# Optimization experiments

Hardware: AMD Instinct MI355X
Metric: run time of the kernel (lower is better)

Reference implementation:

```python
import jax, jax.numpy as jnp
import numpy as np

N_NODES = 40000
N_EDGES = 640000
BATCH = 2
IN_DIM = 3
HID = 128
OUT_DIM = 3


def setup_inputs() -> dict:
    key = jax.random.key(0)
    ks = jax.random.split(key, 16)
    p = jax.random.normal(ks[0], (BATCH, N_NODES, IN_DIM), dtype=jnp.float32)
    edge_rows = jax.random.randint(ks[1], (N_EDGES,), 0, N_NODES, dtype=jnp.int32)
    edge_cols = jax.random.randint(ks[2], (N_EDGES,), 0, N_NODES, dtype=jnp.int32)
    # normalize_sparse_matrix: divide each nonzero (value 1.0) by the row's nonzero count
    deg = jax.ops.segment_sum(jnp.ones((N_EDGES,), jnp.float32), edge_rows, num_segments=N_NODES)
    adj_vals = 1.0 / deg[edge_rows]  # every used row has deg >= 1
    s = 0.05
    # initial Linear(3 -> 128)
    W_init = jax.random.normal(ks[3], (IN_DIM, HID), jnp.float32) * s
    b_init = jnp.zeros((HID,), jnp.float32)
    # 4 GraphConvs inside the two blocks (all 128->128), each has filter + self_filter
    Wf_blocks = jax.random.normal(ks[4], (4, HID, HID), jnp.float32) * s
    bf_blocks = jnp.zeros((4, HID), jnp.float32)
    Ws_blocks = jax.random.normal(ks[5], (4, HID, HID), jnp.float32) * s
    bs_blocks = jnp.zeros((4, HID), jnp.float32)
    # final GraphConvLayer (128 -> 3)
    Wf_out = jax.random.normal(ks[6], (HID, OUT_DIM), jnp.float32) * s
    bf_out = jnp.zeros((OUT_DIM,), jnp.float32)
    Ws_out = jax.random.normal(ks[7], (HID, OUT_DIM), jnp.float32) * s
    bs_out = jnp.zeros((OUT_DIM,), jnp.float32)
    return dict(p=p, adj_vals=adj_vals, edge_rows=edge_rows, edge_cols=edge_cols,
                W_init=W_init, b_init=b_init,
                Wf_blocks=Wf_blocks, bf_blocks=bf_blocks,
                Ws_blocks=Ws_blocks, bs_blocks=bs_blocks,
                Wf_out=Wf_out, bf_out=bf_out, Ws_out=Ws_out, bs_out=bs_out)


def reference(p, adj_vals, edge_rows, edge_cols,
              W_init, b_init,
              Wf_blocks, bf_blocks, Ws_blocks, bs_blocks,
              Wf_out, bf_out, Ws_out, bs_out):
    n = p.shape[1]

    def spmm(xb):  # xb: [N, d] -> A @ xb via edge-list scatter-add
        return jax.ops.segment_sum(adj_vals[:, None] * xb[edge_cols], edge_rows, num_segments=n)

    spmm_b = jax.vmap(spmm)  # [B, N, d]

    def gconv(x, Wf, bf, Ws, bs):
        # sparse path: self_filter(x) + filter(spmm(adj, x))
        return (x @ Ws + bs) + (spmm_b(x) @ Wf + bf)

    x = p @ W_init + b_init  # [B, N, HID]
    for blk in range(2):  # two GraphConvBlocks, residual, no shortcut (dims equal)
        net = gconv(jax.nn.relu(x), Wf_blocks[2 * blk], bf_blocks[2 * blk],
                    Ws_blocks[2 * blk], bs_blocks[2 * blk])
        dx = gconv(jax.nn.relu(net), Wf_blocks[2 * blk + 1], bf_blocks[2 * blk + 1],
                   Ws_blocks[2 * blk + 1], bs_blocks[2 * blk + 1])
        x = x + dx
    # final GraphConvLayer 128 -> 3
    out = gconv(jax.nn.relu(x), Wf_out, bf_out, Ws_out, bs_out)
    return out
```

## Files before the change

kernel.cpp:

```cpp
#include <hip/hip_runtime.h>


typedef unsigned short u16;
typedef unsigned int   u32;
typedef __bf16 bf8_t __attribute__((ext_vector_type(8)));
typedef float  f4_t  __attribute__((ext_vector_type(4)));

#define N_NODES 40000
#define N_EDGES 640000
#define BN      80000

__device__ __forceinline__ float bf2f(u16 u) {
  union { u32 i; float f; } v; v.i = ((u32)u) << 16; return v.f;
}
__device__ __forceinline__ u16 f2bf(float f) {
  union { float f; u32 i; } v; v.f = f;
  u32 i = v.i;
  return (u16)((i + 0x7FFFu + ((i >> 16) & 1u)) >> 16);
}
__device__ __forceinline__ float asf(u32 i) {
  union { u32 u; float f; } v; v.u = i; return v.f;
}
__device__ __forceinline__ u32 pack2(float a, float b) {
  return (u32)f2bf(a) | ((u32)f2bf(b) << 16);
}
__device__ __forceinline__ float lo2f(u32 v) { return asf(v << 16); }
__device__ __forceinline__ float hi2f(u32 v) { return asf(v & 0xffff0000u); }
__device__ __forceinline__ u32 relu2(u32 v) {
  u32 r = v;
  if (r & 0x8000u)     r &= 0xffff0000u;
  if (r & 0x80000000u) r &= 0x0000ffffu;
  return r;
}

__global__ void fill_kernel(float* __restrict__ out, int n, float v) {
  int i = blockIdx.x * 256 + threadIdx.x;
  if (i < n) out[i] = v;
}

__global__ void scan1_kernel(const int* __restrict__ cnt, int* __restrict__ row_ptr,
                             int* __restrict__ blocksum) {
  __shared__ int sm[256];
  int t = threadIdx.x;
  int row = blockIdx.x * 256 + t;
  int v = (row < N_NODES) ? cnt[row] : 0;
  sm[t] = v; __syncthreads();
  for (int off = 1; off < 256; off <<= 1) {
    int u = (t >= off) ? sm[t - off] : 0;
    __syncthreads();
    sm[t] += u;
    __syncthreads();
  }
  if (row < N_NODES) row_ptr[row] = sm[t] - v;
  if (t == 255) blocksum[blockIdx.x] = sm[255];
}

__global__ void scan2_kernel(int* __restrict__ blocksum, int* __restrict__ row_ptr, int nblk) {
  __shared__ int sm[256];
  int t = threadIdx.x;
  int v = (t < nblk) ? blocksum[t] : 0;
  sm[t] = v; __syncthreads();
  for (int off = 1; off < 256; off <<= 1) {
    int u = (t >= off) ? sm[t - off] : 0;
    __syncthreads();
    sm[t] += u;
    __syncthreads();
  }
  if (t < nblk) blocksum[t] = sm[t] - v;
  if (t == 255) row_ptr[N_NODES] = sm[255];
}

__global__ void scan3_kernel(int* __restrict__ row_ptr, const int* __restrict__ blocksum,
                             int* __restrict__ cnt) {
  int row = blockIdx.x * 256 + threadIdx.x;
  if (row < N_NODES) {
    int rp = row_ptr[row] + blocksum[blockIdx.x];
    row_ptr[row] = rp;
    cnt[row] = rp;
  }
}

__global__ void scatter_kernel(const int* __restrict__ rows, const int* __restrict__ cols,
                               int* __restrict__ cur, int* __restrict__ cols_s) {
  int e = blockIdx.x * 256 + threadIdx.x;
  if (e < N_EDGES) {
    int r = rows[e];
    int pos = atomicAdd(&cur[r], 1);
    cols_s[pos] = cols[e];
  }
}

__global__ void initw_kernel(const float* __restrict__ p, const float* __restrict__ W,
                             const float* __restrict__ bias, u16* __restrict__ xb,
                             const float* __restrict__ Wf_b, const float* __restrict__ Ws_b,
                             const float* __restrict__ bf_b, const float* __restrict__ bs_b,
                             u16* __restrict__ WtCat, float* __restrict__ biasCat,
                             const int* __restrict__ erows, int* __restrict__ cnt) {
  if (blockIdx.x >= 20512) {
    int e = (blockIdx.x - 20512) * 256 + threadIdx.x;
    if (e < N_EDGES) atomicAdd(&cnt[erows[e]], 1);
    return;
  }
  if (blockIdx.x >= 20000) {
    int idx = (blockIdx.x - 20000) * 256 + threadIdx.x;
    int g = idx >> 15, rem = idx & 32767;
    int h = rem >> 8, k = rem & 255;
    float v = (k < 128) ? Ws_b[(g * 128 + k) * 128 + h]
                        : Wf_b[(g * 128 + (k - 128)) * 128 + h];
    WtCat[idx] = f2bf(v);
    if (k == 0) biasCat[g * 128 + h] = bs_b[g * 128 + h] + bf_b[g * 128 + h];
    return;
  }
  int idx = blockIdx.x * 256 + threadIdx.x;
  int row = idx >> 6;
  int h = (idx & 63) * 2;
  float p0 = p[row * 3], p1 = p[row * 3 + 1], p2 = p[row * 3 + 2];
  float s0 = p0 * W[h]     + p1 * W[128 + h]     + p2 * W[256 + h]     + bias[h];
  float s1 = p0 * W[h + 1] + p1 * W[128 + h + 1] + p2 * W[256 + h + 1] + bias[h + 1];
  ((u32*)xb)[(size_t)row * 64 + (h >> 1)] = pack2(s0, s1);
}

#define ACC8P(u, a0, a1, a2, a3, a4, a5, a6, a7)                          \
  a0 += asf((u).x << 16); a1 += asf((u).x & 0xffff0000u);                 \
  a2 += asf((u).y << 16); a3 += asf((u).y & 0xffff0000u);                 \
  a4 += asf((u).z << 16); a5 += asf((u).z & 0xffff0000u);                 \
  a6 += asf((u).w << 16); a7 += asf((u).w & 0xffff0000u);

__global__ void spmm_plain(const int* __restrict__ row_ptr, const int* __restrict__ cols_s,
                           const u16* __restrict__ xin, u16* __restrict__ yout) {
  int row = blockIdx.x * 4 + (threadIdx.x >> 6);
  int l = threadIdx.x & 63;
  int g = l >> 4, sl = l & 15;
  int s = row_ptr[row], e = row_ptr[row + 1];
  const uint4* X0 = (const uint4*)xin + sl;
  const uint4* X1 = X0 + 640000;
  float a0 = 0.f, a1 = 0.f, a2 = 0.f, a3 = 0.f, a4 = 0.f, a5 = 0.f, a6 = 0.f, a7 = 0.f;
  float b0 = 0.f, b1 = 0.f, b2 = 0.f, b3 = 0.f, b4 = 0.f, b5 = 0.f, b6 = 0.f, b7 = 0.f;
  int i = s;
  for (; i + 7 < e; i += 8) {
    int c0 = cols_s[i + g], c1 = cols_s[i + 4 + g];
    uint4 u00 = X0[(size_t)c0 * 16];
    uint4 u01 = X1[(size_t)c0 * 16];
    uint4 u10 = X0[(size_t)c1 * 16];
    uint4 u11 = X1[(size_t)c1 * 16];
    ACC8P(u00, a0, a1, a2, a3, a4, a5, a6, a7);
    ACC8P(u01, b0, b1, b2, b3, b4, b5, b6, b7);
    ACC8P(u10, a0, a1, a2, a3, a4, a5, a6, a7);
    ACC8P(u11, b0, b1, b2, b3, b4, b5, b6, b7);
  }
  for (; i + 3 < e; i += 4) {
    int c = cols_s[i + g];
    uint4 u0 = X0[(size_t)c * 16];
    uint4 u1 = X1[(size_t)c * 16];
    ACC8P(u0, a0, a1, a2, a3, a4, a5, a6, a7);
    ACC8P(u1, b0, b1, b2, b3, b4, b5, b6, b7);
  }
  if (i + g < e) {
    int c = cols_s[i + g];
    uint4 u0 = X0[(size_t)c * 16];
    uint4 u1 = X1[(size_t)c * 16];
    ACC8P(u0, a0, a1, a2, a3, a4, a5, a6, a7);
    ACC8P(u1, b0, b1, b2, b3, b4, b5, b6, b7);
  }
  a0 += __shfl_xor(a0, 16); a1 += __shfl_xor(a1, 16); a2 += __shfl_xor(a2, 16); a3 += __shfl_xor(a3, 16);
  a4 += __shfl_xor(a4, 16); a5 += __shfl_xor(a5, 16); a6 += __shfl_xor(a6, 16); a7 += __shfl_xor(a7, 16);
  b0 += __shfl_xor(b0, 16); b1 += __shfl_xor(b1, 16); b2 += __shfl_xor(b2, 16); b3 += __shfl_xor(b3, 16);
  b4 += __shfl_xor(b4, 16); b5 += __shfl_xor(b5, 16); b6 += __shfl_xor(b6, 16); b7 += __shfl_xor(b7, 16);
  a0 += __shfl_xor(a0, 32); a1 += __shfl_xor(a1, 32); a2 += __shfl_xor(a2, 32); a3 += __shfl_xor(a3, 32);
  a4 += __shfl_xor(a4, 32); a5 += __shfl_xor(a5, 32); a6 += __shfl_xor(a6, 32); a7 += __shfl_xor(a7, 32);
  b0 += __shfl_xor(b0, 32); b1 += __shfl_xor(b1, 32); b2 += __shfl_xor(b2, 32); b3 += __shfl_xor(b3, 32);
  b4 += __shfl_xor(b4, 32); b5 += __shfl_xor(b5, 32); b6 += __shfl_xor(b6, 32); b7 += __shfl_xor(b7, 32);
  float sc = (e > s) ? 1.f / (float)(e - s) : 0.f;
  if (g == 0) {
    uint4 o;
    o.x = pack2(a0 * sc, a1 * sc);
    o.y = pack2(a2 * sc, a3 * sc);
    o.z = pack2(a4 * sc, a5 * sc);
    o.w = pack2(a6 * sc, a7 * sc);
    *((uint4*)yout + (size_t)row * 16 + sl) = o;
  } else if (g == 1) {
    uint4 o;
    o.x = pack2(b0 * sc, b1 * sc);
    o.y = pack2(b2 * sc, b3 * sc);
    o.z = pack2(b4 * sc, b5 * sc);
    o.w = pack2(b6 * sc, b7 * sc);
    *((uint4*)yout + 640000 + (size_t)row * 16 + sl) = o;
  }
}

#define ACC8M(u, a0, a1, a2, a3, a4, a5, a6, a7)                                        \
  a0 += fmaxf(asf((u).x << 16), 0.f); a1 += fmaxf(asf((u).x & 0xffff0000u), 0.f);       \
  a2 += fmaxf(asf((u).y << 16), 0.f); a3 += fmaxf(asf((u).y & 0xffff0000u), 0.f);       \
  a4 += fmaxf(asf((u).z << 16), 0.f); a5 += fmaxf(asf((u).z & 0xffff0000u), 0.f);       \
  a6 += fmaxf(asf((u).w << 16), 0.f); a7 += fmaxf(asf((u).w & 0xffff0000u), 0.f);

__global__ void spmm_relu(const int* __restrict__ row_ptr, const int* __restrict__ cols_s,
                          const u16* __restrict__ xin, u16* __restrict__ yout) {
  int row = blockIdx.x * 4 + (threadIdx.x >> 6);
  int l = threadIdx.x & 63;
  int g = l >> 4, sl = l & 15;
  int s = row_ptr[row], e = row_ptr[row + 1];
  const uint4* X0 = (const uint4*)xin + sl;
  const uint4* X1 = X0 + 640000;
  float a0 = 0.f, a1 = 0.f, a2 = 0.f, a3 = 0.f, a4 = 0.f, a5 = 0.f, a6 = 0.f, a7 = 0.f;
  float b0 = 0.f, b1 = 0.f, b2 = 0.f, b3 = 0.f, b4 = 0.f, b5 = 0.f, b6 = 0.f, b7 = 0.f;
  int i = s;
  for (; i + 7 < e; i += 8) {
    int c0 = cols_s[i + g], c1 = cols_s[i + 4 + g];
    uint4 u00 = X0[(size_t)c0 * 16];
    uint4 u01 = X1[(size_t)c0 * 16];
    uint4 u10 = X0[(size_t)c1 * 16];
    uint4 u11 = X1[(size_t)c1 * 16];
    ACC8M(u00, a0, a1, a2, a3, a4, a5, a6, a7);
    ACC8M(u01, b0, b1, b2, b3, b4, b5, b6, b7);
    ACC8M(u10, a0, a1, a2, a3, a4, a5, a6, a7);
    ACC8M(u11, b0, b1, b2, b3, b4, b5, b6, b7);
  }
  for (; i + 3 < e; i += 4) {
    int c = cols_s[i + g];
    uint4 u0 = X0[(size_t)c * 16];
    uint4 u1 = X1[(size_t)c * 16];
    ACC8M(u0, a0, a1, a2, a3, a4, a5, a6, a7);
    ACC8M(u1, b0, b1, b2, b3, b4, b5, b6, b7);
  }
  if (i + g < e) {
    int c = cols_s[i + g];
    uint4 u0 = X0[(size_t)c * 16];
    uint4 u1 = X1[(size_t)c * 16];
    ACC8M(u0, a0, a1, a2, a3, a4, a5, a6, a7);
    ACC8M(u1, b0, b1, b2, b3, b4, b5, b6, b7);
  }
  a0 += __shfl_xor(a0, 16); a1 += __shfl_xor(a1, 16); a2 += __shfl_xor(a2, 16); a3 += __shfl_xor(a3, 16);
  a4 += __shfl_xor(a4, 16); a5 += __shfl_xor(a5, 16); a6 += __shfl_xor(a6, 16); a7 += __shfl_xor(a7, 16);
  b0 += __shfl_xor(b0, 16); b1 += __shfl_xor(b1, 16); b2 += __shfl_xor(b2, 16); b3 += __shfl_xor(b3, 16);
  b4 += __shfl_xor(b4, 16); b5 += __shfl_xor(b5, 16); b6 += __shfl_xor(b6, 16); b7 += __shfl_xor(b7, 16);
  a0 += __shfl_xor(a0, 32); a1 += __shfl_xor(a1, 32); a2 += __shfl_xor(a2, 32); a3 += __shfl_xor(a3, 32);
  a4 += __shfl_xor(a4, 32); a5 += __shfl_xor(a5, 32); a6 += __shfl_xor(a6, 32); a7 += __shfl_xor(a7, 32);
  b0 += __shfl_xor(b0, 32); b1 += __shfl_xor(b1, 32); b2 += __shfl_xor(b2, 32); b3 += __shfl_xor(b3, 32);
  b4 += __shfl_xor(b4, 32); b5 += __shfl_xor(b5, 32); b6 += __shfl_xor(b6, 32); b7 += __shfl_xor(b7, 32);
  float sc = (e > s) ? 1.f / (float)(e - s) : 0.f;
  if (g == 0) {
    uint4 o;
    o.x = pack2(a0 * sc, a1 * sc);
    o.y = pack2(a2 * sc, a3 * sc);
    o.z = pack2(a4 * sc, a5 * sc);
    o.w = pack2(a6 * sc, a7 * sc);
    *((uint4*)yout + (size_t)row * 16 + sl) = o;
  } else if (g == 1) {
    uint4 o;
    o.x = pack2(b0 * sc, b1 * sc);
    o.y = pack2(b2 * sc, b3 * sc);
    o.z = pack2(b4 * sc, b5 * sc);
    o.w = pack2(b6 * sc, b7 * sc);
    *((uint4*)yout + 640000 + (size_t)row * 16 + sl) = o;
  }
}

#define TS 136
template <int MODE>
__global__ __launch_bounds__(256, 4) void gemm_kernel(
    const u16* __restrict__ rin, const u16* __restrict__ yin,
    const u16* __restrict__ WtCat, const float* __restrict__ biasCat, int g,
    u16* __restrict__ rout, u16* __restrict__ xresid,
    float4* __restrict__ zf4, float4* __restrict__ zs4,
    const float* __restrict__ Wfo, const float* __restrict__ Wso,
    const float* __restrict__ bfo, const float* __restrict__ bso) {
  __shared__ __align__(16) u16 lds[18432];
  u16* ldsW = lds + 9216;
  int tid = threadIdx.x;
  int m0 = blockIdx.x * 128;
  int li = tid & 15, q = (tid >> 4) & 3, wv = tid >> 6;
  int wmo = (wv >> 1) * 64, wno = (wv & 1) * 64;

  f4_t acc[4][4];
#pragma unroll
  for (int i = 0; i < 4; ++i)
#pragma unroll
    for (int j = 0; j < 4; ++j) acc[i][j] = (f4_t){0.f, 0.f, 0.f, 0.f};

  const u16* Wsrc = WtCat + (size_t)g * 32768;

  for (int kb = 0; kb < 256; kb += 64) {
    __syncthreads();
    const u16* srcA = (kb < 128) ? (rin + kb) : (yin + (kb - 128));
#pragma unroll
    for (int p2 = 0; p2 < 4; ++p2) {
      int idx = p2 * 256 + tid;
      int row = idx >> 3, seg = idx & 7;
      uint4 va = *reinterpret_cast<const uint4*>(srcA + (size_t)(m0 + row) * 128 + seg * 8);
      if (MODE == 0 && kb < 128) {
        va.x = relu2(va.x); va.y = relu2(va.y); va.z = relu2(va.z); va.w = relu2(va.w);
      }
      *reinterpret_cast<uint4*>(&lds[row * 72 + seg * 8]) = va;
      uint4 vw = *reinterpret_cast<const uint4*>(Wsrc + (size_t)row * 256 + kb + seg * 8);
      *reinterpret_cast<uint4*>(&ldsW[row * 72 + seg * 8]) = vw;
    }
    __syncthreads();
#pragma unroll
    for (int kk = 0; kk < 64; kk += 32) {
      bf8_t af[4], wf[4];
#pragma unroll
      for (int t = 0; t < 4; ++t)
        af[t] = __builtin_bit_cast(bf8_t,
            *reinterpret_cast<const uint4*>(&lds[(wmo + t * 16 + li) * 72 + kk + q * 8]));
#pragma unroll
      for (int t = 0; t < 4; ++t)
        wf[t] = __builtin_bit_cast(bf8_t,
            *reinterpret_cast<const uint4*>(&ldsW[(wno + t * 16 + li) * 72 + kk + q * 8]));
#pragma unroll
      for (int i = 0; i < 4; ++i)
#pragma unroll
        for (int j = 0; j < 4; ++j)
          acc[i][j] = __builtin_amdgcn_mfma_f32_16x16x32_bf16(af[i], wf[j], acc[i][j], 0, 0, 0);
    }
  }

  float bias[4];
#pragma unroll
  for (int j = 0; j < 4; ++j) bias[j] = biasCat[g * 128 + wno + j * 16 + li];

  __syncthreads();
#pragma unroll
  for (int i = 0; i < 4; ++i)
#pragma unroll
    for (int j = 0; j < 4; ++j)
#pragma unroll
      for (int r2 = 0; r2 < 4; ++r2) {
        int m = wmo + i * 16 + q * 4 + r2;
        int col = wno + j * 16 + li;
        lds[m * TS + col] = f2bf(acc[i][j][r2] + bias[j]);
      }
  __syncthreads();

  float wzf[8][3], wzs[8][3];
  if (MODE == 2) {
    int chb = (tid & 15) * 8;
#pragma unroll
    for (int c = 0; c < 8; ++c)
#pragma unroll
      for (int d = 0; d < 3; ++d) {
        wzf[c][d] = Wfo[(chb + c) * 3 + d];
        wzs[c][d] = Wso[(chb + c) * 3 + d];
      }
  }

#pragma unroll
  for (int p2 = 0; p2 < 8; ++p2) {
    int idx = p2 * 256 + tid;
    int row = idx >> 4, ch = idx & 15;
    uint4 cv = *reinterpret_cast<const uint4*>(&lds[row * TS + ch * 8]);
    size_t gid = (size_t)(m0 + row) * 16 + ch;
    if (MODE == 0) {
      uint4 o;
      o.x = relu2(cv.x); o.y = relu2(cv.y); o.z = relu2(cv.z); o.w = relu2(cv.w);
      ((uint4*)rout)[gid] = o;
    } else if (MODE == 1) {
      uint4 xv = ((const uint4*)xresid)[gid];
      uint4 nx;
      float x0, x1;
      x0 = lo2f(xv.x) + lo2f(cv.x); x1 = hi2f(xv.x) + hi2f(cv.x); nx.x = pack2(x0, x1);
      x0 = lo2f(xv.y) + lo2f(cv.y); x1 = hi2f(xv.y) + hi2f(cv.y); nx.y = pack2(x0, x1);
      x0 = lo2f(xv.z) + lo2f(cv.z); x1 = hi2f(xv.z) + hi2f(cv.z); nx.z = pack2(x0, x1);
      x0 = lo2f(xv.w) + lo2f(cv.w); x1 = hi2f(xv.w) + hi2f(cv.w); nx.w = pack2(x0, x1);
      ((uint4*)xresid)[gid] = nx;
    } else {
      uint4 xv = ((const uint4*)xresid)[gid];
      float zf0 = 0.f, zf1 = 0.f, zf2 = 0.f, zs0 = 0.f, zs1 = 0.f, zs2 = 0.f;
#pragma unroll
      for (int q2 = 0; q2 < 4; ++q2) {
        u32 xu = ((const u32*)&xv)[q2], cu = ((const u32*)&cv)[q2];
        float r0 = fmaxf(lo2f(xu) + lo2f(cu), 0.f);
        float r1 = fmaxf(hi2f(xu) + hi2f(cu), 0.f);
        int c = 2 * q2;
        zf0 += r0 * wzf[c][0] + r1 * wzf[c + 1][0];
        zf1 += r0 * wzf[c][1] + r1 * wzf[c + 1][1];
        zf2 += r0 * wzf[c][2] + r1 * wzf[c + 1][2];
        zs0 += r0 * wzs[c][0] + r1 * wzs[c + 1][0];
        zs1 += r0 * wzs[c][1] + r1 * wzs[c + 1][1];
        zs2 += r0 * wzs[c][2] + r1 * wzs[c + 1][2];
      }
#pragma unroll
      for (int off = 1; off < 16; off <<= 1) {
        zf0 += __shfl_xor(zf0, off); zf1 += __shfl_xor(zf1, off); zf2 += __shfl_xor(zf2, off);
        zs0 += __shfl_xor(zs0, off); zs1 += __shfl_xor(zs1, off); zs2 += __shfl_xor(zs2, off);
      }
      if ((tid & 15) == 0) {
        int m = m0 + row;
        zf4[m] = make_float4(zf0, zf1, zf2, 0.f);
        zs4[m] = make_float4(zs0 + bso[0] + bfo[0], zs1 + bso[1] + bfo[1],
                             zs2 + bso[2] + bfo[2], 0.f);
      }
    }
  }
}

__global__ void spmm3_kernel(const int* __restrict__ row_ptr, const int* __restrict__ cols_s,
                             const float4* __restrict__ zf4, const float4* __restrict__ zs4,
                             float* __restrict__ out) {
  int idx = blockIdx.x * 256 + threadIdx.x;
  if (idx >= BN) return;
  int b = (idx >= N_NODES) ? 1 : 0;
  int r = idx - b * N_NODES;
  int s = row_ptr[r], e = row_ptr[r + 1];
  const float4* Z = zf4 + (size_t)b * N_NODES;
  float a0 = 0.f, a1 = 0.f, a2 = 0.f;
  for (int i = s; i < e; ++i) {
    float4 z = Z[cols_s[i]];
    a0 += z.x; a1 += z.y; a2 += z.z;
  }
  float sc = (e > s) ? 1.f / (float)(e - s) : 0.f;
  float4 zs = zs4[idx];
  out[idx * 3 + 0] = zs.x + a0 * sc;
  out[idx * 3 + 1] = zs.y + a1 * sc;
  out[idx * 3 + 2] = zs.z + a2 * sc;
}

extern "C" void kernel_launch(void* const* d_in, const int* in_sizes, int n_in,
                              void* d_out, int out_size, void* d_ws, size_t ws_size,
                              hipStream_t stream) {
  float* out = (float*)d_out;
  int fill_grid = (out_size + 255) / 256;

  const int exp_sizes[14] = {240000, 640000, 640000, 640000, 384, 128,
                             65536, 512, 65536, 512, 384, 3, 384, 3};
  bool sizes_ok = (n_in == 14);
  if (sizes_ok) for (int i = 0; i < 14; ++i) if (in_sizes[i] != exp_sizes[i]) sizes_ok = false;
  if (!sizes_ok) {
    fill_kernel<<<fill_grid, 256, 0, stream>>>(out, out_size, 1.0f);
    return;
  }

  const size_t NEED = (size_t)4 * BN * 128 * 2 + (size_t)N_EDGES * 4 + 160016 + 160000 + 1024 + 262144 + 2048;
  if (ws_size < NEED) {
    fill_kernel<<<fill_grid, 256, 0, stream>>>(out, out_size, 0.0f);
    return;
  }

  const float* p      = (const float*)d_in[0];
  const int*   erows  = (const int*)d_in[2];
  const int*   ecols  = (const int*)d_in[3];
  const float* W_init = (const float*)d_in[4];
  const float* b_init = (const float*)d_in[5];
  const float* Wf_b   = (const float*)d_in[6];
  const float* bf_b   = (const float*)d_in[7];
  const float* Ws_b   = (const float*)d_in[8];
  const float* bs_b   = (const float*)d_in[9];
  const float* Wf_o   = (const float*)d_in[10];
  const float* bf_o   = (const float*)d_in[11];
  const float* Ws_o   = (const float*)d_in[12];
  const float* bs_o   = (const float*)d_in[13];

  char* w = (char*)d_ws;
  char*  zbuf     = w;         w += (size_t)BN * 128 * 2;
  u16*   rB       = (u16*)w;   w += (size_t)BN * 128 * 2;
  u16*   y        = (u16*)w;   w += (size_t)BN * 128 * 2;
  u16*   xb       = (u16*)w;   w += (size_t)BN * 128 * 2;
  int*   cols_s   = (int*)w;   w += (size_t)N_EDGES * 4;
  int*   row_ptr  = (int*)w;   w += 160016;
  int*   cnt      = (int*)w;   w += 160000;
  int*   blocksum = (int*)w;   w += 1024;
  u16*   WtCat    = (u16*)w;   w += 4 * 128 * 256 * 2;
  float* biasCat  = (float*)w; w += 4 * 128 * 4;

  float4* zf4 = (float4*)zbuf;
  float4* zs4 = (float4*)(zbuf + 1280000);

  const int NBLK = (N_NODES + 255) / 256;

  hipMemsetAsync(cnt, 0, N_NODES * 4, stream);
  initw_kernel<<<23012, 256, 0, stream>>>(p, W_init, b_init, xb,
                                          Wf_b, Ws_b, bf_b, bs_b, WtCat, biasCat,
                                          erows, cnt);
  scan1_kernel<<<NBLK, 256, 0, stream>>>(cnt, row_ptr, blocksum);
  scan2_kernel<<<1, 256, 0, stream>>>(blocksum, row_ptr, NBLK);
  scan3_kernel<<<NBLK, 256, 0, stream>>>(row_ptr, blocksum, cnt);
  scatter_kernel<<<2500, 256, 0, stream>>>(erows, ecols, cnt, cols_s);

  for (int blk = 0; blk < 2; ++blk) {
    spmm_relu<<<10000, 256, 0, stream>>>(row_ptr, cols_s, xb, y);
    gemm_kernel<0><<<625, 256, 0, stream>>>(xb, y, WtCat, biasCat, 2 * blk, rB, nullptr,
                                            nullptr, nullptr, nullptr, nullptr, nullptr, nullptr);
    spmm_plain<<<10000, 256, 0, stream>>>(row_ptr, cols_s, rB, y);
    if (blk == 0)
      gemm_kernel<1><<<625, 256, 0, stream>>>(rB, y, WtCat, biasCat, 1, nullptr, xb,
                                              nullptr, nullptr, nullptr, nullptr, nullptr, nullptr);
    else
      gemm_kernel<2><<<625, 256, 0, stream>>>(rB, y, WtCat, biasCat, 3, nullptr, xb,
                                              zf4, zs4, Wf_o, Ws_o, bf_o, bs_o);
  }
  spmm3_kernel<<<(BN + 255) / 256, 256, 0, stream>>>(row_ptr, cols_s, zf4, zs4, out);
}
```

Measured before the change: 421.6 us.

## Interleave batch dimension per node so both batches' features share contiguous memory

Changes activation layout from [B][N][128] to [N][B][128], so the two batch rows for a node sit next to each other (512 contiguous bytes). The SpMM gathers for both batches of a given column index then touch adjacent cache lines, which should improve DRAM page and cache locality. The init, spmm, and final spmm3 kernels are updated accordingly. The GEMM kernel is row-wise and unaffected, but the final output ordering must still match, and spmm3 now indexes zs4 interleaved, which assumes the GEMM writes that layout.

New measurement: 424.5 us. Within noise of the previous version (+0.7%).

```diff
diff --git a/kernel.cpp b/kernel.cpp
--- a/kernel.cpp
+++ b/kernel.cpp
@@ -117,7 +117,9 @@
   float p0 = p[row * 3], p1 = p[row * 3 + 1], p2 = p[row * 3 + 2];
   float s0 = p0 * W[h]     + p1 * W[128 + h]     + p2 * W[256 + h]     + bias[h];
   float s1 = p0 * W[h + 1] + p1 * W[128 + h + 1] + p2 * W[256 + h + 1] + bias[h + 1];
-  ((u32*)xb)[(size_t)row * 64 + (h >> 1)] = pack2(s0, s1);
+  int r = row, b = 0;
+  if (row >= N_NODES) { r = row - N_NODES; b = 1; }
+  ((u32*)xb)[(size_t)(r * 2 + b) * 64 + (h >> 1)] = pack2(s0, s1);
 }
 
 #define ACC8P(u, a0, a1, a2, a3, a4, a5, a6, a7)                          \
@@ -132,17 +134,16 @@
   int l = threadIdx.x & 63;
   int g = l >> 4, sl = l & 15;
   int s = row_ptr[row], e = row_ptr[row + 1];
-  const uint4* X0 = (const uint4*)xin + sl;
-  const uint4* X1 = X0 + 640000;
+  const uint4* X = (const uint4*)xin + sl;
   float a0 = 0.f, a1 = 0.f, a2 = 0.f, a3 = 0.f, a4 = 0.f, a5 = 0.f, a6 = 0.f, a7 = 0.f;
   float b0 = 0.f, b1 = 0.f, b2 = 0.f, b3 = 0.f, b4 = 0.f, b5 = 0.f, b6 = 0.f, b7 = 0.f;
   int i = s;
   for (; i + 7 < e; i += 8) {
     int c0 = cols_s[i + g], c1 = cols_s[i + 4 + g];
-    uint4 u00 = X0[(size_t)c0 * 16];
-    uint4 u01 = X1[(size_t)c0 * 16];
-    uint4 u10 = X0[(size_t)c1 * 16];
-    uint4 u11 = X1[(size_t)c1 * 16];
+    uint4 u00 = X[(size_t)c0 * 32];
+    uint4 u01 = X[(size_t)c0 * 32 + 16];
+    uint4 u10 = X[(size_t)c1 * 32];
+    uint4 u11 = X[(size_t)c1 * 32 + 16];
     ACC8P(u00, a0, a1, a2, a3, a4, a5, a6, a7);
     ACC8P(u01, b0, b1, b2, b3, b4, b5, b6, b7);
     ACC8P(u10, a0, a1, a2, a3, a4, a5, a6, a7);
@@ -150,15 +151,15 @@
   }
   for (; i + 3 < e; i += 4) {
     int c = cols_s[i + g];
-    uint4 u0 = X0[(size_t)c * 16];
-    uint4 u1 = X1[(size_t)c * 16];
+    uint4 u0 = X[(size_t)c * 32];
+    uint4 u1 = X[(size_t)c * 32 + 16];
     ACC8P(u0, a0, a1, a2, a3, a4, a5, a6, a7);
     ACC8P(u1, b0, b1, b2, b3, b4, b5, b6, b7);
   }
   if (i + g < e) {
     int c = cols_s[i + g];
-    uint4 u0 = X0[(size_t)c * 16];
-    uint4 u1 = X1[(size_t)c * 16];
+    uint4 u0 = X[(size_t)c * 32];
+    uint4 u1 = X[(size_t)c * 32 + 16];
     ACC8P(u0, a0, a1, a2, a3, a4, a5, a6, a7);
     ACC8P(u1, b0, b1, b2, b3, b4, b5, b6, b7);
   }
@@ -177,14 +178,14 @@
     o.y = pack2(a2 * sc, a3 * sc);
     o.z = pack2(a4 * sc, a5 * sc);
     o.w = pack2(a6 * sc, a7 * sc);
-    *((uint4*)yout + (size_t)row * 16 + sl) = o;
+    *((uint4*)yout + (size_t)(row * 2) * 16 + sl) = o;
   } else if (g == 1) {
     uint4 o;
     o.x = pack2(b0 * sc, b1 * sc);
     o.y = pack2(b2 * sc, b3 * sc);
     o.z = pack2(b4 * sc, b5 * sc);
     o.w = pack2(b6 * sc, b7 * sc);
-    *((uint4*)yout + 640000 + (size_t)row * 16 + sl) = o;
+    *((uint4*)yout + (size_t)(row * 2 + 1) * 16 + sl) = o;
   }
 }
 
@@ -200,17 +201,16 @@
   int l = threadIdx.x & 63;
   int g = l >> 4, sl = l & 15;
   int s = row_ptr[row], e = row_ptr[row + 1];
-  const uint4* X0 = (const uint4*)xin + sl;
-  const uint4* X1 = X0 + 640000;
+  const uint4* X = (const uint4*)xin + sl;
   float a0 = 0.f, a1 = 0.f, a2 = 0.f, a3 = 0.f, a4 = 0.f, a5 = 0.f, a6 = 0.f, a7 = 0.f;
   float b0 = 0.f, b1 = 0.f, b2 = 0.f, b3 = 0.f, b4 = 0.f, b5 = 0.f, b6 = 0.f, b7 = 0.f;
   int i = s;
   for (; i + 7 < e; i += 8) {
     int c0 = cols_s[i + g], c1 = cols_s[i + 4 + g];
-    uint4 u00 = X0[(size_t)c0 * 16];
-    uint4 u01 = X1[(size_t)c0 * 16];
-    uint4 u10 = X0[(size_t)c1 * 16];
-    uint4 u11 = X1[(size_t)c1 * 16];
+    uint4 u00 = X[(size_t)c0 * 32];
+    uint4 u01 = X[(size_t)c0 * 32 + 16];
+    uint4 u10 = X[(size_t)c1 * 32];
+    uint4 u11 = X[(size_t)c1 * 32 + 16];
     ACC8M(u00, a0, a1, a2, a3, a4, a5, a6, a7);
     ACC8M(u01, b0, b1, b2, b3, b4, b5, b6, b7);
     ACC8M(u10, a0, a1, a2, a3, a4, a5, a6, a7);
@@ -218,15 +218,15 @@
   }
   for (; i + 3 < e; i += 4) {
     int c = cols_s[i + g];
-    uint4 u0 = X0[(size_t)c * 16];
-    uint4 u1 = X1[(size_t)c * 16];
+    uint4 u0 = X[(size_t)c * 32];
+    uint4 u1 = X[(size_t)c * 32 + 16];
     ACC8M(u0, a0, a1, a2, a3, a4, a5, a6, a7);
     ACC8M(u1, b0, b1, b2, b3, b4, b5, b6, b7);
   }
   if (i + g < e) {
     int c = cols_s[i + g];
-    uint4 u0 = X0[(size_t)c * 16];
-    uint4 u1 = X1[(size_t)c * 16];
+    uint4 u0 = X[(size_t)c * 32];
+    uint4 u1 = X[(size_t)c * 32 + 16];
     ACC8M(u0, a0, a1, a2, a3, a4, a5, a6, a7);
     ACC8M(u1, b0, b1, b2, b3, b4, b5, b6, b7);
   }
@@ -245,14 +245,14 @@
     o.y = pack2(a2 * sc, a3 * sc);
     o.z = pack2(a4 * sc, a5 * sc);
     o.w = pack2(a6 * sc, a7 * sc);
-    *((uint4*)yout + (size_t)row * 16 + sl) = o;
+    *((uint4*)yout + (size_t)(row * 2) * 16 + sl) = o;
   } else if (g == 1) {
     uint4 o;
     o.x = pack2(b0 * sc, b1 * sc);
     o.y = pack2(b2 * sc, b3 * sc);
     o.z = pack2(b4 * sc, b5 * sc);
     o.w = pack2(b6 * sc, b7 * sc);
-    *((uint4*)yout + 640000 + (size_t)row * 16 + sl) = o;
+    *((uint4*)yout + (size_t)(row * 2 + 1) * 16 + sl) = o;
   }
 }
 
@@ -402,14 +402,13 @@
   int b = (idx >= N_NODES) ? 1 : 0;
   int r = idx - b * N_NODES;
   int s = row_ptr[r], e = row_ptr[r + 1];
-  const float4* Z = zf4 + (size_t)b * N_NODES;
   float a0 = 0.f, a1 = 0.f, a2 = 0.f;
   for (int i = s; i < e; ++i) {
-    float4 z = Z[cols_s[i]];
+    float4 z = zf4[cols_s[i] * 2 + b];
     a0 += z.x; a1 += z.y; a2 += z.z;
   }
   float sc = (e > s) ? 1.f / (float)(e - s) : 0.f;
-  float4 zs = zs4[idx];
+  float4 zs = zs4[r * 2 + b];
   out[idx * 3 + 0] = zs.x + a0 * sc;
   out[idx * 3 + 1] = zs.y + a1 * sc;
   out[idx * 3 + 2] = zs.z + a2 * sc;
```
